# Performance work log

Measured on AMD Instinct MI355X. Metric: run time of the kernel, lower is better.

The kernel has to match this reference:

```python
import jax, jax.numpy as jnp
import numpy as np

B, T, C, H = 2, 2048, 1024, 16
D = C // H  # head dim, even
NEG = -1e10  # masked_fill value used by the torch module (not -inf)


def _rope_cache(dim, max_positions):
    # Faithful to source: theta_i = 1/10000**(-2*(i-1)/dim), i = arange(dim//2)
    i = jnp.arange(dim // 2, dtype=jnp.float32)
    theta = 1.0 / (10000.0 ** (-2.0 * (i - 1.0) / dim))
    ang = jnp.arange(max_positions, dtype=jnp.float32)[:, None] * theta[None, :]  # [T, D/2]
    return jnp.cos(ang), jnp.sin(ang)


def _apply_rope(x, cos, sin):
    # x: [B,H,T,D]; consecutive pairs form complex numbers (x[...,2j], x[...,2j+1])
    xp = x.reshape(*x.shape[:-1], D // 2, 2)
    xr, xi = xp[..., 0], xp[..., 1]
    rr = xr * cos - xi * sin
    ri = xr * sin + xi * cos
    return jnp.stack([rr, ri], axis=-1).reshape(x.shape)


def setup_inputs() -> dict:
    key = jax.random.key(0)
    ks = jax.random.split(key, 5)
    s = 1.0 / np.sqrt(C)
    return {
        'x': jax.random.normal(ks[0], (B, T, C), jnp.float32),
        'Wq': jax.random.normal(ks[1], (C, C), jnp.float32) * s,
        'bq': jnp.zeros((C,), jnp.float32),
        'Wk': jax.random.normal(ks[2], (C, C), jnp.float32) * s,
        'bk': jnp.zeros((C,), jnp.float32),
        'Wv': jax.random.normal(ks[3], (C, C), jnp.float32) * s,
        'bv': jnp.zeros((C,), jnp.float32),
        'Wp': jax.random.normal(ks[4], (C, C), jnp.float32) * s,
        'bp': jnp.zeros((C,), jnp.float32),
    }


def reference(x, Wq, bq, Wk, bk, Wv, bv, Wp, bp):
    cos, sin = _rope_cache(D, T)  # [T, D/2]
    def split_heads(h):
        return h.reshape(B, T, H, D).transpose(0, 2, 1, 3)  # [B,H,T,D]
    q = split_heads(x @ Wq.T + bq)
    k = split_heads(x @ Wk.T + bk)
    v = split_heads(x @ Wv.T + bv)
    q = _apply_rope(q, cos, sin)
    k = _apply_rope(k, cos, sin)
    att = jnp.einsum('bhqd,bhkd->bhqk', q, k) * (1.0 / np.sqrt(D))  # [B,H,T,T]
    causal = jnp.tril(jnp.ones((T, T), bool))
    att = jnp.where(causal, att, NEG)
    att = jax.nn.softmax(att, axis=-1)
    y = jnp.einsum('bhqk,bhkd->bhqd', att, v)
    y = y.transpose(0, 2, 1, 3).reshape(B, T, C)
    return y @ Wp.T + bp
```

## Files before the change

kernel.cpp:

```cpp
#include <hip/hip_runtime.h>

#define SEQ 2048
#define CDIM 1024
#define NHEAD 16
#define HDIM 64

typedef __bf16 bf16x8 __attribute__((ext_vector_type(8)));
typedef __bf16 bf16x4v __attribute__((ext_vector_type(4)));
typedef float f32x4 __attribute__((ext_vector_type(4)));

typedef const __attribute__((address_space(1))) char* gcp_t;
typedef __attribute__((address_space(3))) char* lcp_t;

__device__ __forceinline__ void gload16(const void* g, void* l) {
    __builtin_amdgcn_global_load_lds((gcp_t)g, (lcp_t)l, 16, 0, 0);
}

__device__ __forceinline__ unsigned short f2bf(float f) {
    unsigned int u = __float_as_uint(f);
    u += 0x7fffu + ((u >> 16) & 1u);
    return (unsigned short)(u >> 16);
}


__global__ void cvt_kernel(const float* __restrict__ src, unsigned short* __restrict__ dst, int n4) {
    int i = blockIdx.x * blockDim.x + threadIdx.x;
    if (i < n4) {
        float4 v = ((const float4*)src)[i];
        ushort4 o;
        o.x = f2bf(v.x); o.y = f2bf(v.y); o.z = f2bf(v.z); o.w = f2bf(v.w);
        ((ushort4*)dst)[i] = o;
    }
}

__global__ void cvtw_kernel(const float* __restrict__ Wq, const float* __restrict__ Wk,
                            const float* __restrict__ Wv, const float* __restrict__ Wp,
                            unsigned short* __restrict__ wqkv, unsigned short* __restrict__ wpb) {
    int i = blockIdx.x * blockDim.x + threadIdx.x;
    int which = i >> 18, r = i & 262143;
    const float* s = (which == 0) ? Wq : (which == 1) ? Wk : (which == 2) ? Wv : Wp;
    unsigned short* d = (which < 3) ? (wqkv + (size_t)which * 1048576) : wpb;
    float4 v = ((const float4*)s)[r];
    ushort4 o;
    o.x = f2bf(v.x); o.y = f2bf(v.y); o.z = f2bf(v.z); o.w = f2bf(v.w);
    ((ushort4*)d)[r] = o;
}

__global__ void rope_kernel(float* __restrict__ ct, float* __restrict__ st) {
    int idx = blockIdx.x * blockDim.x + threadIdx.x;
    int j = idx & 31, t = idx >> 5;
    float e = -2.0f * ((float)j - 1.0f) / 64.0f;
    float denom = (float)pow(10000.0, (double)e);
    float theta = 1.0f / denom;
    float ang = (float)t * theta;
    ct[idx] = cosf(ang);
    st[idx] = sinf(ang);
}

template <int MODE>
__global__ __launch_bounds__(256) void gemm_bt(
    const unsigned short* __restrict__ A, const unsigned short* __restrict__ Bm,
    const float* __restrict__ b0, const float* __restrict__ b1, const float* __restrict__ b2,
    unsigned short* __restrict__ qb, unsigned short* __restrict__ kb,
    unsigned short* __restrict__ vtb, float* __restrict__ outf,
    const float* __restrict__ ctab, const float* __restrict__ stab)
{
    constexpr int K = 1024;
    __shared__ __align__(16) unsigned short As[128 * 32];
    __shared__ __align__(16) unsigned short Bs[128 * 32];
    const int tid = threadIdx.x, lane = tid & 63, wid = tid >> 6;
    const int m0 = blockIdx.y * 128, n0 = blockIdx.x * 128;
    const int wr = wid >> 1, wc = wid & 1;

    f32x4 acc[4][4] = {};

    const char* Ag = (const char*)(A + (size_t)m0 * K);
    const char* Bg = (const char*)(Bm + (size_t)n0 * K);
    const int r0 = tid >> 2, cb = (tid & 3) * 16;
    const int r1 = r0 + 64;
    const int ldsw = wid << 10;
    char* AsB = (char*)As;
    char* BsB = (char*)Bs;

    for (int k0 = 0; k0 < K; k0 += 32) {
        gload16(Ag + (size_t)r0 * 2048 + k0 * 2 + cb, AsB + ldsw);
        gload16(Ag + (size_t)r1 * 2048 + k0 * 2 + cb, AsB + 4096 + ldsw);
        gload16(Bg + (size_t)r0 * 2048 + k0 * 2 + cb, BsB + ldsw);
        gload16(Bg + (size_t)r1 * 2048 + k0 * 2 + cb, BsB + 4096 + ldsw);
        __syncthreads();
        bf16x8 af[4], bfr[4];
#pragma unroll
        for (int am = 0; am < 4; ++am)
            af[am] = *(const bf16x8*)(As + (wr * 64 + am * 16 + (lane & 15)) * 32 + (lane >> 4) * 8);
#pragma unroll
        for (int an = 0; an < 4; ++an)
            bfr[an] = *(const bf16x8*)(Bs + (wc * 64 + an * 16 + (lane & 15)) * 32 + (lane >> 4) * 8);
#pragma unroll
        for (int am = 0; am < 4; ++am)
#pragma unroll
            for (int an = 0; an < 4; ++an)
                acc[am][an] = __builtin_amdgcn_mfma_f32_16x16x32_bf16(af[am], bfr[an], acc[am][an], 0, 0, 0);
        __syncthreads();
    }

    if (MODE == 0) {
        const float QSCL = 0.18033688011112042f;
#pragma unroll
        for (int an = 0; an < 4; ++an) {
            const int ng = n0 + wc * 64 + an * 16 + (lane & 15);
            const int which = ng >> 10, nl = ng & 1023;
            const int h = nl >> 6, d = nl & 63;
            const float* bptr = (which == 0) ? b0 : (which == 1) ? b1 : b2;
            const float bias = bptr[nl];
            if (which < 2) {
                unsigned short* dst = (which == 0) ? qb : kb;
                const float qs = (which == 0) ? QSCL : 1.0f;
                const int j = d >> 1;
#pragma unroll
                for (int am = 0; am < 4; ++am) {
#pragma unroll
                    for (int i = 0; i < 4; ++i) {
                        const int row = m0 + wr * 64 + am * 16 + (lane >> 4) * 4 + i;
                        const int bb = row >> 11, t = row & 2047;
                        float v = acc[am][an][i] + bias;
                        float p = __shfl_xor(v, 1);
                        const float cv = ctab[t * 32 + j];
                        const float sv = stab[t * 32 + j];
                        v = (d & 1) ? fmaf(v, cv, p * sv) : fmaf(v, cv, -p * sv);
                        dst[((size_t)((bb * 16 + h) * 2048 + t)) * 64 + d] = f2bf(v * qs);
                    }
                }
            } else {
#pragma unroll
                for (int am = 0; am < 4; ++am) {
                    const int rowb = m0 + wr * 64 + am * 16 + (lane >> 4) * 4;
                    const int bb = rowb >> 11, t = rowb & 2047;
                    ushort4 pk;
                    pk.x = f2bf(acc[am][an][0] + bias);
                    pk.y = f2bf(acc[am][an][1] + bias);
                    pk.z = f2bf(acc[am][an][2] + bias);
                    pk.w = f2bf(acc[am][an][3] + bias);
                    *(ushort4*)(vtb + ((size_t)((bb * 16 + h) * 64 + d)) * 2048 + t) = pk;
                }
            }
        }
    } else {
#pragma unroll
        for (int an = 0; an < 4; ++an) {
            const int col = n0 + wc * 64 + an * 16 + (lane & 15);
            const float bias = b0[col];
#pragma unroll
            for (int am = 0; am < 4; ++am)
#pragma unroll
                for (int i = 0; i < 4; ++i) {
                    const int row = m0 + wr * 64 + am * 16 + (lane >> 4) * 4 + i;
                    outf[(size_t)row * 1024 + col] = acc[am][an][i] + bias;
                }
        }
    }
}

__global__ __launch_bounds__(256) void attn_kernel(
    const unsigned short* __restrict__ qb, const unsigned short* __restrict__ kb,
    const unsigned short* __restrict__ vtb, unsigned short* __restrict__ yb)
{
    __shared__ __align__(16) unsigned short Ks[2][64 * 64];
    __shared__ __align__(16) unsigned short Vs[2][64 * 64];
    __shared__ __align__(16) unsigned short Ps[4][16 * 64];
    const int tid = threadIdx.x, lane = tid & 63, wid = tid >> 6;
    const int bh = blockIdx.y;
    const int b = bh >> 4, h = bh & 15;
    const int qt = (bh & 16) ? (31 - blockIdx.x) : blockIdx.x;
    const int q0 = qt * 64;
    const int qw = q0 + wid * 16;
    const unsigned short* Qg = qb + (size_t)bh * SEQ * HDIM;
    const char* Kg = (const char*)(kb + (size_t)bh * SEQ * HDIM);
    const char* Vg = (const char*)(vtb + (size_t)bh * HDIM * SEQ);

    bf16x8 qf[2];
#pragma unroll
    for (int kf = 0; kf < 2; ++kf)
        qf[kf] = *(const bf16x8*)(Qg + (size_t)(qw + (lane & 15)) * 64 + kf * 32 + (lane >> 4) * 8);

    f32x4 o[4] = {};
    float mrun = -3e38f;
    float lrun = 0.0f;

    const int nt = qt + 1;
    const int cr0 = tid >> 3, cc0 = ((tid & 7) * 16) ^ ((cr0 & 7) << 4);
    const int cr1 = cr0 + 32, cc1 = ((tid & 7) * 16) ^ ((cr1 & 7) << 4);
    const int ldsw = wid << 10;

    auto stage = [&](int kt, int bufi) {
        const size_t kv0 = (size_t)kt * 64;
        gload16(Kg + (kv0 + cr0) * 128 + cc0, (char*)Ks[bufi] + ldsw);
        gload16(Kg + (kv0 + cr1) * 128 + cc1, (char*)Ks[bufi] + 4096 + ldsw);
        gload16(Vg + (size_t)cr0 * 4096 + kv0 * 2 + cc0, (char*)Vs[bufi] + ldsw);
        gload16(Vg + (size_t)cr1 * 4096 + kv0 * 2 + cc1, (char*)Vs[bufi] + 4096 + ldsw);
    };

    stage(0, 0);
    __syncthreads();

    for (int kt = 0; kt < nt; ++kt) {
        const int cur = kt & 1;
        if (kt + 1 < nt) stage(kt + 1, cur ^ 1);
        const int kv0 = kt * 64;
        {
            f32x4 s[4] = {};
            __builtin_amdgcn_s_setprio(1);
#pragma unroll
            for (int kf = 0; kf < 2; ++kf) {
                bf16x8 kfr[4];
#pragma unroll
                for (int an = 0; an < 4; ++an) {
                    const int r = an * 16 + (lane & 15);
                    kfr[an] = *(const bf16x8*)((const char*)Ks[cur] + r * 128 + ((kf * 64 + (lane >> 4) * 16) ^ ((r & 7) << 4)));
                }
#pragma unroll
                for (int an = 0; an < 4; ++an)
                    s[an] = __builtin_amdgcn_mfma_f32_16x16x32_bf16(kfr[an], qf[kf], s[an], 0, 0, 0);
            }
            __builtin_amdgcn_s_setprio(0);
            const bool need_mask = (kv0 + 63 > qw);
            const int qg = qw + (lane & 15);
            const int kbase = kv0 + ((lane >> 4) << 2);
            float p[4][4];
            float mx = -3e38f;
#pragma unroll
            for (int an = 0; an < 4; ++an)
#pragma unroll
                for (int i = 0; i < 4; ++i) {
                    float v = s[an][i];
                    if (need_mask && (kbase + an * 16 + i > qg)) v = -3e38f;
                    p[an][i] = v;
                    mx = fmaxf(mx, v);
                }
            mx = fmaxf(mx, __shfl_xor(mx, 16));
            mx = fmaxf(mx, __shfl_xor(mx, 32));
            if (!__all(mx <= mrun + 8.0f)) {
                const float mnew = fmaxf(mrun, mx);
                const float fsc = __builtin_amdgcn_exp2f(mrun - mnew);
                lrun *= fsc;
#pragma unroll
                for (int dn = 0; dn < 4; ++dn) o[dn] *= fsc;
                mrun = mnew;
            }
            float rs = 0.0f;
#pragma unroll
            for (int an = 0; an < 4; ++an)
#pragma unroll
                for (int i = 0; i < 4; ++i) {
                    p[an][i] = __builtin_amdgcn_exp2f(p[an][i] - mrun);
                    rs += p[an][i];
                }
            rs += __shfl_xor(rs, 16);
            rs += __shfl_xor(rs, 32);
            lrun += rs;
            const int ql = lane & 15;
            char* pb = (char*)Ps[wid] + ql * 128;
            const int xr = (ql & 7) << 4;
            const int gb = (lane >> 4) << 3;
#pragma unroll
            for (int an = 0; an < 4; ++an) {
                bf16x4v pk;
                pk[0] = (__bf16)p[an][0]; pk[1] = (__bf16)p[an][1];
                pk[2] = (__bf16)p[an][2]; pk[3] = (__bf16)p[an][3];
                *(bf16x4v*)(pb + ((an * 32 + gb) ^ xr)) = pk;
            }
            __builtin_amdgcn_s_setprio(1);
#pragma unroll
            for (int kf = 0; kf < 2; ++kf) {
                bf16x8 vf[4], pf;
#pragma unroll
                for (int dn = 0; dn < 4; ++dn) {
                    const int r = dn * 16 + (lane & 15);
                    vf[dn] = *(const bf16x8*)((const char*)Vs[cur] + r * 128 + ((kf * 64 + (lane >> 4) * 16) ^ ((r & 7) << 4)));
                }
                {
                    const int qlr = lane & 15;
                    pf = *(const bf16x8*)((const char*)Ps[wid] + qlr * 128 + ((kf * 64 + (lane >> 4) * 16) ^ ((qlr & 7) << 4)));
                }
#pragma unroll
                for (int dn = 0; dn < 4; ++dn)
                    o[dn] = __builtin_amdgcn_mfma_f32_16x16x32_bf16(vf[dn], pf, o[dn], 0, 0, 0);
            }
            __builtin_amdgcn_s_setprio(0);
        }
        __syncthreads();
    }

    {
        const float inv = 1.0f / lrun;
        const int qg = qw + (lane & 15);
        unsigned short* yrow = yb + (size_t)(b * SEQ + qg) * CDIM + h * 64;
#pragma unroll
        for (int dn = 0; dn < 4; ++dn) {
            const int d = dn * 16 + ((lane >> 4) << 2);
            bf16x4v pk;
            pk[0] = (__bf16)(o[dn][0] * inv);
            pk[1] = (__bf16)(o[dn][1] * inv);
            pk[2] = (__bf16)(o[dn][2] * inv);
            pk[3] = (__bf16)(o[dn][3] * inv);
            *(bf16x4v*)(yrow + d) = pk;
        }
    }
}


extern "C" void kernel_launch(void* const* d_in, const int* in_sizes, int n_in,
                              void* d_out, int out_size, void* d_ws, size_t ws_size,
                              hipStream_t stream) {
    (void)in_sizes; (void)n_in; (void)out_size; (void)ws_size;
    const float* x  = (const float*)d_in[0];
    const float* Wq = (const float*)d_in[1];
    const float* bq = (const float*)d_in[2];
    const float* Wk = (const float*)d_in[3];
    const float* bk = (const float*)d_in[4];
    const float* Wv = (const float*)d_in[5];
    const float* bv = (const float*)d_in[6];
    const float* Wp = (const float*)d_in[7];
    const float* bp = (const float*)d_in[8];
    float* out = (float*)d_out;

    char* ws = (char*)d_ws;
    size_t off = 0;
    auto take = [&](size_t bytes) -> char* {
        char* p = ws + off;
        off = (off + bytes + 255) & ~(size_t)255;
        return p;
    };
    float* ctab = (float*)take((size_t)SEQ * 32 * 4);
    float* stab = (float*)take((size_t)SEQ * 32 * 4);
    unsigned short* xb   = (unsigned short*)take((size_t)4096 * 1024 * 2);
    unsigned short* wqkv = (unsigned short*)take((size_t)3 * 1024 * 1024 * 2);
    unsigned short* wpb  = (unsigned short*)take((size_t)1024 * 1024 * 2);
    unsigned short* qbuf = (unsigned short*)take((size_t)32 * SEQ * HDIM * 2);
    unsigned short* kbuf = (unsigned short*)take((size_t)32 * SEQ * HDIM * 2);
    unsigned short* vtb  = (unsigned short*)take((size_t)32 * HDIM * SEQ * 2);
    unsigned short* yb   = (unsigned short*)take((size_t)4096 * 1024 * 2);

    rope_kernel<<<256, 256, 0, stream>>>(ctab, stab);
    cvt_kernel<<<4096, 256, 0, stream>>>(x, xb, 1048576);
    cvtw_kernel<<<4096, 256, 0, stream>>>(Wq, Wk, Wv, Wp, wqkv, wpb);

    dim3 g0(24, 32);
    gemm_bt<0><<<g0, 256, 0, stream>>>(xb, wqkv, bq, bk, bv, qbuf, kbuf, vtb, nullptr, ctab, stab);
    dim3 g1(32, 32);
    attn_kernel<<<g1, 256, 0, stream>>>(qbuf, kbuf, vtb, yb);
    dim3 g2(8, 32);
    gemm_bt<1><<<g2, 256, 0, stream>>>(yb, wpb, bp, nullptr, nullptr, nullptr, nullptr, nullptr, out, nullptr, nullptr);
}
```

Measured before the change: 144.8 us.

## Double-buffer GEMM LDS tiles and interleave RoPE cos/sin table

The GEMM's K loop now uses two LDS buffers for A and B. The global-to-LDS load for the next K slice is issued before the MFMA work on the current slice, so global memory latency can overlap with compute instead of stalling on a barrier each iteration. The RoPE cos and sin tables are merged into one interleaved float2 table, so each element in the QKV epilogue needs one 8-byte load instead of two separate loads. Double buffering doubles the GEMM's LDS use, which may lower occupancy.

Result: faster. 139.5 us (-3.7%).

```diff
diff --git a/kernel.cpp b/kernel.cpp
--- a/kernel.cpp
+++ b/kernel.cpp
@@ -46,15 +46,14 @@
     ((ushort4*)d)[r] = o;
 }
 
-__global__ void rope_kernel(float* __restrict__ ct, float* __restrict__ st) {
+__global__ void rope_kernel(float2* __restrict__ cstab) {
     int idx = blockIdx.x * blockDim.x + threadIdx.x;
     int j = idx & 31, t = idx >> 5;
     float e = -2.0f * ((float)j - 1.0f) / 64.0f;
     float denom = (float)pow(10000.0, (double)e);
     float theta = 1.0f / denom;
     float ang = (float)t * theta;
-    ct[idx] = cosf(ang);
-    st[idx] = sinf(ang);
+    cstab[idx] = make_float2(cosf(ang), sinf(ang));
 }
 
 template <int MODE>
@@ -63,11 +62,12 @@
     const float* __restrict__ b0, const float* __restrict__ b1, const float* __restrict__ b2,
     unsigned short* __restrict__ qb, unsigned short* __restrict__ kb,
     unsigned short* __restrict__ vtb, float* __restrict__ outf,
-    const float* __restrict__ ctab, const float* __restrict__ stab)
+    const float2* __restrict__ cstab)
 {
     constexpr int K = 1024;
-    __shared__ __align__(16) unsigned short As[128 * 32];
-    __shared__ __align__(16) unsigned short Bs[128 * 32];
+    constexpr int NIT = K / 32;
+    __shared__ __align__(16) unsigned short As[2][128 * 32];
+    __shared__ __align__(16) unsigned short Bs[2][128 * 32];
     const int tid = threadIdx.x, lane = tid & 63, wid = tid >> 6;
     const int m0 = blockIdx.y * 128, n0 = blockIdx.x * 128;
     const int wr = wid >> 1, wc = wid & 1;
@@ -79,22 +79,27 @@
     const int r0 = tid >> 2, cb = (tid & 3) * 16;
     const int r1 = r0 + 64;
     const int ldsw = wid << 10;
-    char* AsB = (char*)As;
-    char* BsB = (char*)Bs;
-
-    for (int k0 = 0; k0 < K; k0 += 32) {
-        gload16(Ag + (size_t)r0 * 2048 + k0 * 2 + cb, AsB + ldsw);
-        gload16(Ag + (size_t)r1 * 2048 + k0 * 2 + cb, AsB + 4096 + ldsw);
-        gload16(Bg + (size_t)r0 * 2048 + k0 * 2 + cb, BsB + ldsw);
-        gload16(Bg + (size_t)r1 * 2048 + k0 * 2 + cb, BsB + 4096 + ldsw);
-        __syncthreads();
+
+    auto stage = [&](int k0, int bufi) {
+        gload16(Ag + (size_t)r0 * 2048 + k0 * 2 + cb, (char*)As[bufi] + ldsw);
+        gload16(Ag + (size_t)r1 * 2048 + k0 * 2 + cb, (char*)As[bufi] + 4096 + ldsw);
+        gload16(Bg + (size_t)r0 * 2048 + k0 * 2 + cb, (char*)Bs[bufi] + ldsw);
+        gload16(Bg + (size_t)r1 * 2048 + k0 * 2 + cb, (char*)Bs[bufi] + 4096 + ldsw);
+    };
+
+    stage(0, 0);
+    __syncthreads();
+
+    for (int it = 0; it < NIT; ++it) {
+        const int cur = it & 1;
+        if (it + 1 < NIT) stage((it + 1) * 32, cur ^ 1);
         bf16x8 af[4], bfr[4];
 #pragma unroll
         for (int am = 0; am < 4; ++am)
-            af[am] = *(const bf16x8*)(As + (wr * 64 + am * 16 + (lane & 15)) * 32 + (lane >> 4) * 8);
+            af[am] = *(const bf16x8*)(As[cur] + (wr * 64 + am * 16 + (lane & 15)) * 32 + (lane >> 4) * 8);
 #pragma unroll
         for (int an = 0; an < 4; ++an)
-            bfr[an] = *(const bf16x8*)(Bs + (wc * 64 + an * 16 + (lane & 15)) * 32 + (lane >> 4) * 8);
+            bfr[an] = *(const bf16x8*)(Bs[cur] + (wc * 64 + an * 16 + (lane & 15)) * 32 + (lane >> 4) * 8);
 #pragma unroll
         for (int am = 0; am < 4; ++am)
 #pragma unroll
@@ -124,9 +129,8 @@
                         const int bb = row >> 11, t = row & 2047;
                         float v = acc[am][an][i] + bias;
                         float p = __shfl_xor(v, 1);
-                        const float cv = ctab[t * 32 + j];
-                        const float sv = stab[t * 32 + j];
-                        v = (d & 1) ? fmaf(v, cv, p * sv) : fmaf(v, cv, -p * sv);
+                        const float2 cs = cstab[t * 32 + j];
+                        v = (d & 1) ? fmaf(v, cs.x, p * cs.y) : fmaf(v, cs.x, -p * cs.y);
                         dst[((size_t)((bb * 16 + h) * 2048 + t)) * 64 + d] = f2bf(v * qs);
                     }
                 }
@@ -330,8 +334,7 @@
         off = (off + bytes + 255) & ~(size_t)255;
         return p;
     };
-    float* ctab = (float*)take((size_t)SEQ * 32 * 4);
-    float* stab = (float*)take((size_t)SEQ * 32 * 4);
+    float2* cstab = (float2*)take((size_t)SEQ * 32 * 8);
     unsigned short* xb   = (unsigned short*)take((size_t)4096 * 1024 * 2);
     unsigned short* wqkv = (unsigned short*)take((size_t)3 * 1024 * 1024 * 2);
     unsigned short* wpb  = (unsigned short*)take((size_t)1024 * 1024 * 2);
@@ -340,14 +343,14 @@
     unsigned short* vtb  = (unsigned short*)take((size_t)32 * HDIM * SEQ * 2);
     unsigned short* yb   = (unsigned short*)take((size_t)4096 * 1024 * 2);
 
-    rope_kernel<<<256, 256, 0, stream>>>(ctab, stab);
+    rope_kernel<<<256, 256, 0, stream>>>(cstab);
     cvt_kernel<<<4096, 256, 0, stream>>>(x, xb, 1048576);
     cvtw_kernel<<<4096, 256, 0, stream>>>(Wq, Wk, Wv, Wp, wqkv, wpb);
 
     dim3 g0(24, 32);
-    gemm_bt<0><<<g0, 256, 0, stream>>>(xb, wqkv, bq, bk, bv, qbuf, kbuf, vtb, nullptr, ctab, stab);
+    gemm_bt<0><<<g0, 256, 0, stream>>>(xb, wqkv, bq, bk, bv, qbuf, kbuf, vtb, nullptr, cstab);
     dim3 g1(32, 32);
     attn_kernel<<<g1, 256, 0, stream>>>(qbuf, kbuf, vtb, yb);
     dim3 g2(8, 32);
-    gemm_bt<1><<<g2, 256, 0, stream>>>(yb, wpb, bp, nullptr, nullptr, nullptr, nullptr, nullptr, out, nullptr, nullptr);
-}
+    gemm_bt<1><<<g2, 256, 0, stream>>>(yb, wpb, bp, nullptr, nullptr, nullptr, nullptr, nullptr, out, cstab);
+}
```
